# Optimization experiments

Measured on AMD Instinct MI355X. Metric: run time of the kernel, lower is better.

## Reference

```python
import jax, jax.numpy as jnp
import numpy as np

B, T, U, H, M, K, C = 64, 800, 80, 512, 20, 10, 80  # batch, tsteps, char len, rnn_size, nmixtures, kmixtures, char_vec_len


def _lstm(x, W, Uw, b):
    """Keras-semantics LSTM (gate order i,f,g,o), zero initial state. x: [B,T,D] -> [B,T,H]."""
    xg = jnp.einsum('btd,dh->bth', x, W) + b  # precompute input contribution
    h0 = jnp.zeros((x.shape[0], Uw.shape[0]), x.dtype)
    c0 = jnp.zeros_like(h0)

    def step(carry, zt):
        h, c = carry
        z = zt + h @ Uw
        i, f, g, o = jnp.split(z, 4, axis=-1)
        c = jax.nn.sigmoid(f) * c + jax.nn.sigmoid(i) * jnp.tanh(g)
        h = jax.nn.sigmoid(o) * jnp.tanh(c)
        return (h, c), h

    _, hs = jax.lax.scan(step, (h0, c0), jnp.swapaxes(xg, 0, 1))
    return jnp.swapaxes(hs, 0, 1)


def _forward(stroke_data, char_seq, kappa0, W0, U0, b0, W1, U1, b1, W2, U2, b2, Wa, ba, Wm, bm):
    lstm0_out = _lstm(stroke_data, W0, U0, b0)  # [B,T,H]
    # Attention window: the per-timestep loop in the source only carries kappa,
    # which is a running sum of exp(kappa_offset) -> vectorize via cumsum.
    abk = jnp.exp(jnp.einsum('bth,hk->btk', lstm0_out, Wa) + ba)  # [B,T,3K]
    alpha, beta, koff = jnpp_split = jnp.split(abk, 3, axis=-1)
    kappa = kappa0[:, None, :, 0] + jnp.cumsum(koff, axis=1)  # [B,T,K]
    u = jnp.arange(char_seq.shape[1], dtype=stroke_data.dtype)  # [U]
    # phi: [B,T,U] = sum_k alpha * exp(-beta * (kappa - u)^2)
    phi = jnp.sum(alpha[..., None] * jnp.exp(-beta[..., None] * (kappa[..., None] - u) ** 2), axis=2)
    windows = jnp.einsum('btu,buc->btc', phi, char_seq)  # [B,T,C]
    aug = jnp.concatenate([lstm0_out, windows, stroke_data], axis=-1)
    lstm1_out = _lstm(aug, W1, U1, b1)
    lstm2_out = _lstm(lstm1_out, W2, U2, b2)
    mdn = jnp.einsum('bth,hn->btn', lstm2_out, Wm) + bm  # [B,T,1+6M]
    eos_hat = mdn[..., 0:1]
    pi_hat, mu1, mu2, s1_hat, s2_hat, rho_hat = jnp.split(mdn[..., 1:], 6, axis=-1)
    return jnp.concatenate([
        jax.nn.sigmoid(-eos_hat),
        jax.nn.softmax(pi_hat, axis=-1),
        mu1, mu2,
        jnp.exp(s1_hat), jnp.exp(s2_hat),
        jnp.tanh(rho_hat),
    ], axis=-1)  # [B,T,1+6M]


def setup_inputs() -> dict:
    key = jax.random.key(0)
    ks = jax.random.split(key, 12)
    init = lambda k, shape: jax.random.truncated_normal(k, -2.0, 2.0, shape, jnp.float32) * 0.075
    return {
        'stroke_data': jax.random.normal(ks[0], (B, T, 3), jnp.float32),
        'char_seq': jax.nn.one_hot(jax.random.randint(ks[1], (B, U), 0, C), C, dtype=jnp.float32),
        'kappa0': jnp.zeros((B, K, 1), jnp.float32),
        'W0': init(ks[2], (3, 4 * H)), 'U0': init(ks[3], (H, 4 * H)), 'b0': jnp.zeros((4 * H,)),
        'W1': init(ks[4], (H + C + 3, 4 * H)), 'U1': init(ks[5], (H, 4 * H)), 'b1': jnp.zeros((4 * H,)),
        'W2': init(ks[6], (H, 4 * H)), 'U2': init(ks[7], (H, 4 * H)), 'b2': jnp.zeros((4 * H,)),
        'Wa': init(ks[8], (H, 3 * K)),
        'ba': -3.0 + 0.25 * jax.random.truncated_normal(ks[9], -2.0, 2.0, (3 * K,), jnp.float32),
        'Wm': init(ks[10], (H, 1 + 6 * M)), 'bm': jnp.zeros((1 + 6 * M,)),
    }


def reference(stroke_data, char_seq, kappa0, W0, U0, b0, W1, U1, b1, W2, U2, b2, Wa, ba, Wm, bm):
    return _forward(stroke_data, char_seq, kappa0, W0, U0, b0, W1, U1, b1, W2, U2, b2, Wa, ba, Wm, bm)
```

## Files before the change

### kernel.cpp

```cpp
#include <hip/hip_runtime.h>

typedef unsigned short u16;
typedef unsigned int u32;
typedef short v8s __attribute__((ext_vector_type(8)));
typedef float v4f __attribute__((ext_vector_type(4)));
typedef unsigned int v4u __attribute__((ext_vector_type(4)));
typedef unsigned int v2u __attribute__((ext_vector_type(2)));

#define MFMA16 __builtin_amdgcn_mfma_f32_16x16x32_bf16

constexpr int TT = 800;
constexpr int NBLK = 178;

constexpr int AUGB  = 2240;
constexpr int AUG2B = 2048;

constexpr size_t AUGR_OFF  = 16384;
constexpr size_t AUG2R_OFF = AUGR_OFF + (size_t)4 * 64 * AUGB;
constexpr size_t WAT_OFF   = AUG2R_OFF + (size_t)4 * 64 * AUG2B;
constexpr size_t WS_ZERO   = WAT_OFF + (size_t)32 * 512 * 2;

constexpr u32 SMEM_BYTES = 82944;

__device__ __forceinline__ float bf2f(u16 u) { return __uint_as_float(((u32)u) << 16); }
__device__ __forceinline__ u16 f2bf(float f) {
    u32 x = __float_as_uint(f);
    return (u16)((x + 0x7fffu + ((x >> 16) & 1u)) >> 16);
}
__device__ __forceinline__ short f2bfs(float f) { return (short)f2bf(f); }
__device__ __forceinline__ float sigf(float x) { return 1.f / (1.f + __expf(-x)); }
__device__ __forceinline__ float tanhf2(float x) { return 1.f - 2.f / (1.f + __expf(2.f * x)); }

__device__ __forceinline__ __amdgpu_buffer_rsrc_t mkrsrc(const void* p) {
    return __builtin_amdgcn_make_buffer_rsrc((void*)p, (short)0, -1, 0x00020000);
}
__device__ __forceinline__ v4u ldu4(__amdgpu_buffer_rsrc_t r, int off) {
    return __builtin_amdgcn_raw_buffer_load_b128(r, off, 0, 17);
}
__device__ __forceinline__ void stq8(__amdgpu_buffer_rsrc_t r, int off, u16 a, u16 b, u16 c, u16 d) {
    v2u t; t[0] = (u32)a | ((u32)b << 16); t[1] = (u32)c | ((u32)d << 16);
    __builtin_amdgcn_raw_buffer_store_b64(t, r, off, 0, 17);
}
__device__ __forceinline__ void stq4(__amdgpu_buffer_rsrc_t r, int off, u16 a, u16 b) {
    u32 t = (u32)a | ((u32)b << 16);
    __builtin_amdgcn_raw_buffer_store_b32(t, r, off, 0, 17);
}

__device__ __forceinline__ void gbar(u32* ctrl, u32 target) {
    __syncthreads();
    if (threadIdx.x == 0) {
        u32 old = __hip_atomic_fetch_add(ctrl, 1u, __ATOMIC_RELAXED, __HIP_MEMORY_SCOPE_AGENT);
        if (old == target * NBLK - 1) {
            #pragma unroll
            for (int k = 0; k < 32; k++)
                __hip_atomic_store(ctrl + 1024 + k * 64, target, __ATOMIC_RELAXED, __HIP_MEMORY_SCOPE_AGENT);
        } else {
            u32* gen = ctrl + 1024 + (blockIdx.x & 31) * 64;
            int sp = 0;
            while (__hip_atomic_load(gen, __ATOMIC_RELAXED, __HIP_MEMORY_SCOPE_AGENT) < target) {
                if (sp >= 2) __builtin_amdgcn_s_sleep(8);
                else if (sp == 1) __builtin_amdgcn_s_sleep(1);
                sp++;
            }
        }
    }
    __syncthreads();
}

__global__ void wat_init(const float* __restrict__ Wa, u16* __restrict__ WaT) {
    __amdgpu_buffer_rsrc_t r = mkrsrc(WaT);
    for (int idx = blockIdx.x * 256 + threadIdx.x; idx < 32 * 512 / 2; idx += gridDim.x * 256) {
        const int e0 = idx * 2, e1 = e0 + 1;
        const int n0 = e0 >> 9, k0 = e0 & 511;
        const int n1 = e1 >> 9, k1 = e1 & 511;
        const u16 a = (n0 < 30) ? f2bf(Wa[k0 * 30 + n0]) : (u16)0;
        const u16 b = (n1 < 30) ? f2bf(Wa[k1 * 30 + n1]) : (u16)0;
        stq4(r, idx * 4, a, b);
    }
}

__global__ __launch_bounds__(256, 1) void hw_main(
    const float* __restrict__ stroke, const float* __restrict__ charseq, const float* __restrict__ kappa0,
    const float* __restrict__ W0, const float* __restrict__ U0, const float* __restrict__ b0,
    const float* __restrict__ W1, const float* __restrict__ U1, const float* __restrict__ b1,
    const float* __restrict__ W2, const float* __restrict__ U2, const float* __restrict__ b2,
    const float* __restrict__ ba, const float* __restrict__ Wm, const float* __restrict__ bm,
    float* __restrict__ out, char* __restrict__ ws)
{
    extern __shared__ __align__(16) char smem[];
    u32* ctrl = (u32*)ws;
    u16* augr  = (u16*)(ws + AUGR_OFF);
    u16* aug2r = (u16*)(ws + AUG2R_OFF);
    const u16* WaT = (const u16*)(ws + WAT_OFF);

    const int blk = blockIdx.x, tid = threadIdx.x;
    const int wave = tid >> 6, lane = tid & 63;
    const int quad = lane >> 4, l15 = lane & 15;

    if (blk < 32) {
        const int cs = blk & 15, mg = blk >> 4;
        __amdgpu_buffer_rsrc_t ra = mkrsrc(augr);
        u16*   aL  = (u16*)smem;
        float* zb  = (float*)(smem + 33280);
        float* w0s = (float*)(smem + 50176);
        float* b0s = (float*)(smem + 51712);
        if (tid < 128) {
            const int cn2 = (tid >> 5) * 512 + cs * 32 + (tid & 31);
            b0s[tid] = b0[cn2];
            #pragma unroll
            for (int d = 0; d < 3; d++) w0s[d * 128 + tid] = W0[d * 2048 + cn2];
        }
        v8s bw0[16], bw1[16];
        {
            const int cnA = wave * 512 + cs * 32 + l15;
            const int cnB = cnA + 16;
            #pragma unroll
            for (int kc = 0; kc < 16; kc++)
                #pragma unroll
                for (int j = 0; j < 8; j++) {
                    const int k = kc * 32 + quad * 8 + j;
                    bw0[kc][j] = f2bfs(U0[k * 2048 + cnA]);
                    bw1[kc][j] = f2bfs(U0[k * 2048 + cnB]);
                }
        }
        float cst[4] = {0.f, 0.f, 0.f, 0.f};
        __syncthreads();
        #pragma unroll 1
        for (int i = 0; i <= TT + 3; i++) {
            if (i < TT) {
                const int t = i;
                {
                    const int base = (((t + 3) & 3) * 64 + mg * 32) * AUGB;
                    #pragma unroll
                    for (int c8 = 0; c8 < 8; c8++) {
                        const int c = tid + 256 * c8;
                        const int row = c >> 6, off = c & 63;
                        v4u d = ldu4(ra, base + row * AUGB + off * 16);
                        *(v4u*)((char*)aL + row * 1040 + off * 16) = d;
                    }
                }
                __syncthreads();
                v4f c0a = {0,0,0,0}, c0b = {0,0,0,0}, c1a = {0,0,0,0}, c1b = {0,0,0,0};
                const int xo = quad * 16;
                #pragma unroll
                for (int kc = 0; kc < 16; kc++) {
                    v8s x0 = *(const v8s*)((const char*)aL + l15 * 1040 + kc * 64 + xo);
                    v8s x1 = *(const v8s*)((const char*)aL + (16 + l15) * 1040 + kc * 64 + xo);
                    c0a = MFMA16(x0, bw0[kc], c0a, 0, 0, 0);
                    c1a = MFMA16(x0, bw1[kc], c1a, 0, 0, 0);
                    c0b = MFMA16(x1, bw0[kc], c0b, 0, 0, 0);
                    c1b = MFMA16(x1, bw1[kc], c1b, 0, 0, 0);
                }
                const int n0 = wave * 32 + l15, n1 = n0 + 16;
                #pragma unroll
                for (int r = 0; r < 4; r++) {
                    zb[(quad * 4 + r) * 132 + n0] = c0a[r];
                    zb[(quad * 4 + r) * 132 + n1] = c1a[r];
                    zb[(16 + quad * 4 + r) * 132 + n0] = c0b[r];
                    zb[(16 + quad * 4 + r) * 132 + n1] = c1b[r];
                }
                __syncthreads();
                {
                    const int bl = tid & 31, jj = tid >> 5;
                    const int b = mg * 32 + bl;
                    const float xx0 = stroke[(b * TT + t) * 3 + 0];
                    const float xx1 = stroke[(b * TT + t) * 3 + 1];
                    const float xx2 = stroke[(b * TT + t) * 3 + 2];
                    u16 hv[4];
                    #pragma unroll
                    for (int m = 0; m < 4; m++) {
                        const int j = jj * 4 + m;
                        float z[4];
                        #pragma unroll
                        for (int g = 0; g < 4; g++) {
                            const int n = g * 32 + j;
                            z[g] = zb[bl * 132 + n] + b0s[n] + xx0 * w0s[n] + xx1 * w0s[128 + n] + xx2 * w0s[256 + n];
                        }
                        const float cc = sigf(z[1]) * cst[m] + sigf(z[0]) * tanhf2(z[2]);
                        cst[m] = cc;
                        hv[m] = f2bf(sigf(z[3]) * tanhf2(cc));
                    }
                    stq8(ra, ((t & 3) * 64 + b) * AUGB + (cs * 32 + jj * 4) * 2, hv[0], hv[1], hv[2], hv[3]);
                }
            }
            if (i < TT + 3) gbar(ctrl, (u32)(i + 1));
        }
    } else if (blk < 96) {
        const int q = blk - 32, cs = q >> 1, mg = q & 1;
        __amdgpu_buffer_rsrc_t ra = mkrsrc(augr);
        __amdgpu_buffer_rsrc_t r2 = mkrsrc(aug2r);
        u16*   aL  = (u16*)smem;
        float* zb  = (float*)(smem + 72192);
        float* b1s = (float*)(smem + 80896);
        if (tid < 64) b1s[tid] = b1[(tid >> 4) * 512 + cs * 16 + (tid & 15)];
        v8s bw[35];
        {
            const int cn = wave * 512 + cs * 16 + l15;
            #pragma unroll
            for (int kc = 0; kc < 35; kc++)
                #pragma unroll
                for (int j = 0; j < 8; j++) {
                    const int k = kc * 32 + quad * 8 + j;
                    short v = 0;
                    if (k < 595) v = f2bfs(W1[k * 2048 + cn]);
                    else if (k >= 596 && k < 1108) v = f2bfs(U1[(k - 596) * 2048 + cn]);
                    bw[kc][j] = v;
                }
        }
        float cst[2] = {0.f, 0.f};
        __syncthreads();
        #pragma unroll 1
        for (int i = 0; i <= TT + 3; i++) {
            if (i >= 2 && i <= TT + 1) {
                const int t1 = i - 2;
                {
                    const int base = ((t1 & 3) * 64 + mg * 32) * AUGB;
                    #pragma unroll
                    for (int c18 = 0; c18 < 18; c18++) {
                        const int c = tid + 256 * c18;
                        if (c < 4480) {
                            const int row = c / 140, off = c - row * 140;
                            v4u d = ldu4(ra, base + row * AUGB + off * 16);
                            *(v4u*)((char*)aL + row * 2256 + off * 16) = d;
                        }
                    }
                }
                __syncthreads();
                v4f c0 = {0,0,0,0}, c1 = {0,0,0,0};
                const int xo = quad * 16;
                #pragma unroll
                for (int kc = 0; kc < 35; kc++) {
                    v8s x0 = *(const v8s*)((const char*)aL + l15 * 2256 + kc * 64 + xo);
                    v8s x1 = *(const v8s*)((const char*)aL + (16 + l15) * 2256 + kc * 64 + xo);
                    c0 = MFMA16(x0, bw[kc], c0, 0, 0, 0);
                    c1 = MFMA16(x1, bw[kc], c1, 0, 0, 0);
                }
                #pragma unroll
                for (int r = 0; r < 4; r++) {
                    zb[(quad * 4 + r) * 68 + wave * 17 + l15] = c0[r];
                    zb[(16 + quad * 4 + r) * 68 + wave * 17 + l15] = c1[r];
                }
                __syncthreads();
                {
                    const int bl = tid & 31, jj = tid >> 5;
                    const int b = mg * 32 + bl;
                    u16 hv[2];
                    #pragma unroll
                    for (int m = 0; m < 2; m++) {
                        const int j = jj * 2 + m;
                        float z[4];
                        #pragma unroll
                        for (int g = 0; g < 4; g++)
                            z[g] = zb[bl * 68 + g * 17 + j] + b1s[g * 16 + j];
                        const float cc = sigf(z[1]) * cst[m] + sigf(z[0]) * tanhf2(z[2]);
                        cst[m] = cc;
                        hv[m] = f2bf(sigf(z[3]) * tanhf2(cc));
                    }
                    stq4(ra, (((t1 + 1) & 3) * 64 + b) * AUGB + (596 + cs * 16 + jj * 2) * 2, hv[0], hv[1]);
                    stq4(r2, ((t1 & 3) * 64 + b) * AUG2B + (cs * 16 + jj * 2) * 2, hv[0], hv[1]);
                }
            }
            if (i < TT + 3) gbar(ctrl, (u32)(i + 1));
        }
    } else if (blk < 160) {
        const int q = blk - 96, cs = q >> 1, mg = q & 1;
        __amdgpu_buffer_rsrc_t r2 = mkrsrc(aug2r);
        u16*   aL  = (u16*)smem;
        float* zb  = (float*)(smem + 66048);
        float* b2s = (float*)(smem + 74752);
        if (tid < 64) b2s[tid] = b2[(tid >> 4) * 512 + cs * 16 + (tid & 15)];
        v8s bw[32];
        {
            const int cn = wave * 512 + cs * 16 + l15;
            #pragma unroll
            for (int kc = 0; kc < 32; kc++)
                #pragma unroll
                for (int j = 0; j < 8; j++) {
                    const int k = kc * 32 + quad * 8 + j;
                    bw[kc][j] = (k < 512) ? f2bfs(W2[k * 2048 + cn]) : f2bfs(U2[(k - 512) * 2048 + cn]);
                }
        }
        float cst[2] = {0.f, 0.f};
        __syncthreads();
        #pragma unroll 1
        for (int i = 0; i <= TT + 3; i++) {
            if (i >= 3 && i <= TT + 2) {
                const int t2 = i - 3;
                {
                    const int base = ((t2 & 3) * 64 + mg * 32) * AUG2B;
                    #pragma unroll
                    for (int c16 = 0; c16 < 16; c16++) {
                        const int c = tid + 256 * c16;
                        const int row = c >> 7, off = c & 127;
                        v4u d = ldu4(r2, base + row * AUG2B + off * 16);
                        *(v4u*)((char*)aL + row * 2064 + off * 16) = d;
                    }
                }
                __syncthreads();
                v4f c0 = {0,0,0,0}, c1 = {0,0,0,0};
                const int xo = quad * 16;
                #pragma unroll
                for (int kc = 0; kc < 32; kc++) {
                    v8s x0 = *(const v8s*)((const char*)aL + l15 * 2064 + kc * 64 + xo);
                    v8s x1 = *(const v8s*)((const char*)aL + (16 + l15) * 2064 + kc * 64 + xo);
                    c0 = MFMA16(x0, bw[kc], c0, 0, 0, 0);
                    c1 = MFMA16(x1, bw[kc], c1, 0, 0, 0);
                }
                #pragma unroll
                for (int r = 0; r < 4; r++) {
                    zb[(quad * 4 + r) * 68 + wave * 17 + l15] = c0[r];
                    zb[(16 + quad * 4 + r) * 68 + wave * 17 + l15] = c1[r];
                }
                __syncthreads();
                {
                    const int bl = tid & 31, jj = tid >> 5;
                    const int b = mg * 32 + bl;
                    u16 hv[2];
                    #pragma unroll
                    for (int m = 0; m < 2; m++) {
                        const int j = jj * 2 + m;
                        float z[4];
                        #pragma unroll
                        for (int g = 0; g < 4; g++)
                            z[g] = zb[bl * 68 + g * 17 + j] + b2s[g * 16 + j];
                        const float cc = sigf(z[1]) * cst[m] + sigf(z[0]) * tanhf2(z[2]);
                        cst[m] = cc;
                        hv[m] = f2bf(sigf(z[3]) * tanhf2(cc));
                    }
                    stq4(r2, (((t2 + 1) & 3) * 64 + b) * AUG2B + (512 + cs * 16 + jj * 2) * 2, hv[0], hv[1]);
                }
            }
            if (i < TT + 3) gbar(ctrl, (u32)(i + 1));
        }
    } else if (blk < 176) {
        const int a = blk - 160;
        const int b = a * 4 + wave;
        __amdgpu_buffer_rsrc_t ra = mkrsrc(augr);
        u16*   watl = (u16*)smem;
        u16*   hrow = (u16*)(smem + 33280);
        float* phis = (float*)(smem + 37440);
        u16*   idxs = (u16*)(smem + 38720);
        {
            #pragma unroll
            for (int c8 = 0; c8 < 8; c8++) {
                const int c = tid + 256 * c8;
                const int row = c >> 6, off = c & 63;
                *(v4u*)((char*)watl + row * 1040 + off * 16) = *(const v4u*)(WaT + row * 512 + off * 8);
            }
        }
        #pragma unroll
        for (int rep = 0; rep < 2; rep++) {
            const int u = rep * 64 + lane;
            if (u < 80) {
                int c = 0;
                #pragma unroll 1
                for (int cc = 0; cc < 80; cc++)
                    if (charseq[b * 6400 + u * 80 + cc] > 0.5f) c = cc;
                idxs[wave * 80 + u] = (u16)c;
            }
        }
        float kap = (lane < 10) ? kappa0[b * 10 + lane] : 0.f;
        const float baf = (lane < 30) ? ba[lane] : 0.f;
        const int nn = lane & 31;
        const int k0 = (lane >> 5) * 256;
        const u16* wrow = watl + nn * 520 + k0;
        __syncthreads();
        #pragma unroll 1
        for (int i = 0; i <= TT + 3; i++) {
            if (i >= 1 && i <= TT) {
                const int ta = i - 1;
                {
                    const int row = tid >> 6, off = tid & 63;
                    v4u d = ldu4(ra, ((ta & 3) * 64 + a * 4 + row) * AUGB + off * 16);
                    *(v4u*)((char*)hrow + row * 1040 + off * 16) = d;
                }
                __syncthreads();
                float acc = 0.f;
                #pragma unroll
                for (int kk = 0; kk < 32; kk++) {
                    v8s hv = *(const v8s*)((const char*)hrow + wave * 1040 + (k0 + kk * 8) * 2);
                    v8s wv = *(const v8s*)(wrow + kk * 8);
                    #pragma unroll
                    for (int e = 0; e < 8; e++) acc += bf2f((u16)hv[e]) * bf2f((u16)wv[e]);
                }
                acc += __shfl_xor(acc, 32);
                const float abk = __expf(acc + baf);
                const float kofv = __shfl(abk, 20 + (lane < 10 ? lane : 0));
                if (lane < 10) kap += kofv;
                const float u1f = (float)lane, u2f = (float)(64 + lane);
                float p1 = 0.f, p2 = 0.f;
                #pragma unroll
                for (int kk = 0; kk < 10; kk++) {
                    const float al = __shfl(abk, kk);
                    const float be = __shfl(abk, 10 + kk);
                    const float kp = __shfl(kap, kk);
                    const float d1 = kp - u1f, d2 = kp - u2f;
                    p1 += al * __expf(-be * d1 * d1);
                    p2 += al * __expf(-be * d2 * d2);
                }
                phis[wave * 80 + lane] = p1;
                if (lane < 16) phis[wave * 80 + 64 + lane] = p2;
                __syncthreads();
                const int db = (((ta & 3) * 64 + b) * AUGB) + 512 * 2;
                if (lane < 40) {
                    const int c0 = 2 * lane;
                    float w0 = 0.f, w1 = 0.f;
                    #pragma unroll 1
                    for (int u = 0; u < 80; u++) {
                        const float pv = phis[wave * 80 + u];
                        const int ix = (int)idxs[wave * 80 + u];
                        w0 += (ix == c0)     ? pv : 0.f;
                        w1 += (ix == c0 + 1) ? pv : 0.f;
                    }
                    stq4(ra, db + c0 * 2, f2bf(w0), f2bf(w1));
                } else if (lane == 40) {
                    stq4(ra, db + 80 * 2, f2bf(stroke[(b * TT + ta) * 3 + 0]), f2bf(stroke[(b * TT + ta) * 3 + 1]));
                } else if (lane == 41) {
                    stq4(ra, db + 82 * 2, f2bf(stroke[(b * TT + ta) * 3 + 2]), (u16)0);
                }
            }
            if (i < TT + 3) gbar(ctrl, (u32)(i + 1));
        }
    } else if (blk < 178) {
        const int mgs = blk - 176;
        __amdgpu_buffer_rsrc_t r2 = mkrsrc(aug2r);
        u16*   aL = (u16*)smem;
        float* zb = (float*)(smem + 33280);
        v8s bw0[16], bw1[16];
        {
            const int nA = wave * 32 + l15, nB = nA + 16;
            #pragma unroll
            for (int kc = 0; kc < 16; kc++)
                #pragma unroll
                for (int j = 0; j < 8; j++) {
                    const int k = kc * 32 + quad * 8 + j;
                    bw0[kc][j] = (nA < 121) ? f2bfs(Wm[k * 121 + nA]) : (short)0;
                    bw1[kc][j] = (nB < 121) ? f2bfs(Wm[k * 121 + nB]) : (short)0;
                }
        }
        __syncthreads();
        #pragma unroll 1
        for (int i = 0; i <= TT + 3; i++) {
            if (i >= 4) {
                const int tm = i - 4;
                {
                    const int base = (((tm + 1) & 3) * 64 + mgs * 32) * AUG2B + 1024;
                    #pragma unroll
                    for (int c8 = 0; c8 < 8; c8++) {
                        const int c = tid + 256 * c8;
                        const int row = c >> 6, off = c & 63;
                        v4u d = ldu4(r2, base + row * AUG2B + off * 16);
                        *(v4u*)((char*)aL + row * 1040 + off * 16) = d;
                    }
                }
                __syncthreads();
                v4f c0a = {0,0,0,0}, c0b = {0,0,0,0}, c1a = {0,0,0,0}, c1b = {0,0,0,0};
                const int xo = quad * 16;
                #pragma unroll
                for (int kc = 0; kc < 16; kc++) {
                    v8s x0 = *(const v8s*)((const char*)aL + l15 * 1040 + kc * 64 + xo);
                    v8s x1 = *(const v8s*)((const char*)aL + (16 + l15) * 1040 + kc * 64 + xo);
                    c0a = MFMA16(x0, bw0[kc], c0a, 0, 0, 0);
                    c1a = MFMA16(x0, bw1[kc], c1a, 0, 0, 0);
                    c0b = MFMA16(x1, bw0[kc], c0b, 0, 0, 0);
                    c1b = MFMA16(x1, bw1[kc], c1b, 0, 0, 0);
                }
                const int n0 = wave * 32 + l15, n1 = n0 + 16;
                #pragma unroll
                for (int r = 0; r < 4; r++) {
                    zb[(quad * 4 + r) * 132 + n0] = c0a[r];
                    zb[(quad * 4 + r) * 132 + n1] = c1a[r];
                    zb[(16 + quad * 4 + r) * 132 + n0] = c0b[r];
                    zb[(16 + quad * 4 + r) * 132 + n1] = c1b[r];
                }
                __syncthreads();
                {
                    const int b8 = tid >> 3, g8 = tid & 7;
                    const int b = mgs * 32 + b8;
                    const float* zr = zb + b8 * 132;
                    float* orow = out + ((size_t)(b * TT + tm)) * 121;
                    if (g8 == 0) {
                        orow[0] = sigf(-(zr[0] + bm[0]));
                        float mx = -1e30f;
                        float zv[20];
                        #pragma unroll 1
                        for (int nl = 1; nl <= 20; nl++) { zv[nl - 1] = zr[nl] + bm[nl]; mx = fmaxf(mx, zv[nl - 1]); }
                        float ss = 0.f;
                        #pragma unroll 1
                        for (int nl = 0; nl < 20; nl++) { zv[nl] = __expf(zv[nl] - mx); ss += zv[nl]; }
                        const float inv = 1.f / ss;
                        #pragma unroll 1
                        for (int nl = 0; nl < 20; nl++) orow[nl + 1] = zv[nl] * inv;
                    } else if (g8 <= 2) {
                        const int s0 = 21 + (g8 - 1) * 20;
                        #pragma unroll 1
                        for (int nl = s0; nl < s0 + 20; nl++) orow[nl] = zr[nl] + bm[nl];
                    } else if (g8 <= 4) {
                        const int s0 = 61 + (g8 - 3) * 20;
                        #pragma unroll 1
                        for (int nl = s0; nl < s0 + 20; nl++) orow[nl] = __expf(zr[nl] + bm[nl]);
                    } else if (g8 <= 6) {
                        const int s0 = 101 + (g8 - 5) * 10;
                        #pragma unroll 1
                        for (int nl = s0; nl < s0 + 10; nl++) orow[nl] = tanhf2(zr[nl] + bm[nl]);
                    }
                }
            }
            if (i < TT + 3) gbar(ctrl, (u32)(i + 1));
        }
    }
}

extern "C" void kernel_launch(void* const* d_in, const int* in_sizes, int n_in,
                              void* d_out, int out_size, void* d_ws, size_t ws_size,
                              hipStream_t stream) {
    const float* stroke  = (const float*)d_in[0];
    const float* charseq = (const float*)d_in[1];
    const float* kappa0  = (const float*)d_in[2];
    const float* W0 = (const float*)d_in[3];
    const float* U0 = (const float*)d_in[4];
    const float* b0 = (const float*)d_in[5];
    const float* W1 = (const float*)d_in[6];
    const float* U1 = (const float*)d_in[7];
    const float* b1 = (const float*)d_in[8];
    const float* W2 = (const float*)d_in[9];
    const float* U2 = (const float*)d_in[10];
    const float* b2 = (const float*)d_in[11];
    const float* Wa = (const float*)d_in[12];
    const float* ba = (const float*)d_in[13];
    const float* Wm = (const float*)d_in[14];
    const float* bm = (const float*)d_in[15];
    char* ws = (char*)d_ws;

    static bool attr_done = false;
    if (!attr_done) {
        hipFuncSetAttribute((const void*)hw_main,
                            hipFuncAttributeMaxDynamicSharedMemorySize, SMEM_BYTES);
        attr_done = true;
    }

    hipMemsetAsync(d_ws, 0, WS_ZERO, stream);
    wat_init<<<8, 256, 0, stream>>>(Wa, (u16*)(ws + WAT_OFF));
    hw_main<<<NBLK, 256, SMEM_BYTES, stream>>>(stroke, charseq, kappa0, W0, U0, b0,
                                               W1, U1, b1, W2, U2, b2, ba, Wm, bm,
                                               (float*)d_out, ws);
}
```

Measured before the change: 10.46 ms.

## Replace global lockstep barrier with per-stage dataflow counters between pipeline stages

Removes the grid-wide barrier that forced all 178 blocks to advance one step together. Each stage now publishes per-timestep completion counters, and before each step it waits only on the specific producer and consumer counters it depends on (done and read flags for a 4-slot ring). Stages can run ahead of each other and the critical recurrent path is no longer stalled by the slowest unrelated block. In exchange there are more atomics and polling per step, and the ring-buffer dependency logic has to be exactly right to avoid races.

Result: faster. 8.690 ms (-16.9%).

```diff
diff --git a/kernel.cpp b/kernel.cpp
--- a/kernel.cpp
+++ b/kernel.cpp
@@ -15,12 +15,14 @@
 constexpr int AUGB  = 2240;
 constexpr int AUG2B = 2048;
 
-constexpr size_t AUGR_OFF  = 16384;
+constexpr size_t AUGR_OFF  = 131072;
 constexpr size_t AUG2R_OFF = AUGR_OFF + (size_t)4 * 64 * AUGB;
 constexpr size_t WAT_OFF   = AUG2R_OFF + (size_t)4 * 64 * AUG2B;
 constexpr size_t WS_ZERO   = WAT_OFF + (size_t)32 * 512 * 2;
 
 constexpr u32 SMEM_BYTES = 82944;
+
+enum { G_S0D = 0, G_SAD = 1, G_S1D = 2, G_S2D = 3, G_S1R = 4, G_SAR = 5, G_S2R = 6, G_SMR = 7 };
 
 __device__ __forceinline__ float bf2f(u16 u) { return __uint_as_float(((u32)u) << 16); }
 __device__ __forceinline__ u16 f2bf(float f) {
@@ -46,22 +48,34 @@
     __builtin_amdgcn_raw_buffer_store_b32(t, r, off, 0, 17);
 }
 
-__device__ __forceinline__ void gbar(u32* ctrl, u32 target) {
-    __syncthreads();
-    if (threadIdx.x == 0) {
-        u32 old = __hip_atomic_fetch_add(ctrl, 1u, __ATOMIC_RELAXED, __HIP_MEMORY_SCOPE_AGENT);
-        if (old == target * NBLK - 1) {
-            #pragma unroll
-            for (int k = 0; k < 32; k++)
-                __hip_atomic_store(ctrl + 1024 + k * 64, target, __ATOMIC_RELAXED, __HIP_MEMORY_SCOPE_AGENT);
-        } else {
-            u32* gen = ctrl + 1024 + (blockIdx.x & 31) * 64;
-            int sp = 0;
-            while (__hip_atomic_load(gen, __ATOMIC_RELAXED, __HIP_MEMORY_SCOPE_AGENT) < target) {
-                if (sp >= 2) __builtin_amdgcn_s_sleep(8);
-                else if (sp == 1) __builtin_amdgcn_s_sleep(1);
-                sp++;
-            }
+__device__ __forceinline__ void publish(u32* ctrl, int g, int t, int blk) {
+    __hip_atomic_fetch_add(ctrl + g * 4096 + (t & 3) * 1024 + (blk & 15) * 64, 1u,
+                           __ATOMIC_RELAXED, __HIP_MEMORY_SCOPE_AGENT);
+}
+__device__ __forceinline__ void wait4(u32* ctrl,
+    int g0, int t0, u32 n0, int g1, int t1, u32 n1,
+    int g2, int t2, u32 n2, int g3, int t3, u32 n3)
+{
+    if (threadIdx.x < 64) {
+        const int lane = threadIdx.x;
+        const int cl = lane >> 4, k = lane & 15;
+        int g, tt; u32 nn;
+        if (cl == 0)      { g = g0; tt = t0; nn = n0; }
+        else if (cl == 1) { g = g1; tt = t1; nn = n1; }
+        else if (cl == 2) { g = g2; tt = t2; nn = n2; }
+        else              { g = g3; tt = t3; nn = n3; }
+        const u32 tgt = (g >= 0 && tt >= 0) ? nn * (u32)((tt >> 2) + 1) : 0u;
+        u32* p = (tgt > 0) ? (ctrl + g * 4096 + (tt & 3) * 1024 + k * 64) : (u32*)0;
+        int sp = 0;
+        for (;;) {
+            u32 v = p ? __hip_atomic_load(p, __ATOMIC_RELAXED, __HIP_MEMORY_SCOPE_AGENT) : 0u;
+            v += __shfl_xor(v, 1); v += __shfl_xor(v, 2);
+            v += __shfl_xor(v, 4); v += __shfl_xor(v, 8);
+            const bool bad = (tgt > 0) && (v < tgt);
+            if (__ballot(bad) == 0ull) break;
+            if (sp >= 2) __builtin_amdgcn_s_sleep(4);
+            else if (sp == 1) __builtin_amdgcn_s_sleep(1);
+            sp++;
         }
     }
     __syncthreads();
@@ -126,64 +140,63 @@
         float cst[4] = {0.f, 0.f, 0.f, 0.f};
         __syncthreads();
         #pragma unroll 1
-        for (int i = 0; i <= TT + 3; i++) {
-            if (i < TT) {
-                const int t = i;
-                {
-                    const int base = (((t + 3) & 3) * 64 + mg * 32) * AUGB;
+        for (int t = 0; t < TT; t++) {
+            wait4(ctrl, G_S0D, t - 1, 32, G_S1R, t - 4, 64, G_SAR, t - 4, 16, -1, 0, 0);
+            {
+                const int base = (((t + 3) & 3) * 64 + mg * 32) * AUGB;
+                #pragma unroll
+                for (int c8 = 0; c8 < 8; c8++) {
+                    const int c = tid + 256 * c8;
+                    const int row = c >> 6, off = c & 63;
+                    v4u d = ldu4(ra, base + row * AUGB + off * 16);
+                    *(v4u*)((char*)aL + row * 1040 + off * 16) = d;
+                }
+            }
+            __syncthreads();
+            v4f c0a = {0,0,0,0}, c0b = {0,0,0,0}, c1a = {0,0,0,0}, c1b = {0,0,0,0};
+            const int xo = quad * 16;
+            #pragma unroll
+            for (int kc = 0; kc < 16; kc++) {
+                v8s x0 = *(const v8s*)((const char*)aL + l15 * 1040 + kc * 64 + xo);
+                v8s x1 = *(const v8s*)((const char*)aL + (16 + l15) * 1040 + kc * 64 + xo);
+                c0a = MFMA16(x0, bw0[kc], c0a, 0, 0, 0);
+                c1a = MFMA16(x0, bw1[kc], c1a, 0, 0, 0);
+                c0b = MFMA16(x1, bw0[kc], c0b, 0, 0, 0);
+                c1b = MFMA16(x1, bw1[kc], c1b, 0, 0, 0);
+            }
+            const int n0 = wave * 32 + l15, n1 = n0 + 16;
+            #pragma unroll
+            for (int r = 0; r < 4; r++) {
+                zb[(quad * 4 + r) * 132 + n0] = c0a[r];
+                zb[(quad * 4 + r) * 132 + n1] = c1a[r];
+                zb[(16 + quad * 4 + r) * 132 + n0] = c0b[r];
+                zb[(16 + quad * 4 + r) * 132 + n1] = c1b[r];
+            }
+            __syncthreads();
+            {
+                const int bl = tid & 31, jj = tid >> 5;
+                const int b = mg * 32 + bl;
+                const float xx0 = stroke[(b * TT + t) * 3 + 0];
+                const float xx1 = stroke[(b * TT + t) * 3 + 1];
+                const float xx2 = stroke[(b * TT + t) * 3 + 2];
+                u16 hv[4];
+                #pragma unroll
+                for (int m = 0; m < 4; m++) {
+                    const int j = jj * 4 + m;
+                    float z[4];
                     #pragma unroll
-                    for (int c8 = 0; c8 < 8; c8++) {
-                        const int c = tid + 256 * c8;
-                        const int row = c >> 6, off = c & 63;
-                        v4u d = ldu4(ra, base + row * AUGB + off * 16);
-                        *(v4u*)((char*)aL + row * 1040 + off * 16) = d;
+                    for (int g = 0; g < 4; g++) {
+                        const int n = g * 32 + j;
+                        z[g] = zb[bl * 132 + n] + b0s[n] + xx0 * w0s[n] + xx1 * w0s[128 + n] + xx2 * w0s[256 + n];
                     }
-                }
-                __syncthreads();
-                v4f c0a = {0,0,0,0}, c0b = {0,0,0,0}, c1a = {0,0,0,0}, c1b = {0,0,0,0};
-                const int xo = quad * 16;
-                #pragma unroll
-                for (int kc = 0; kc < 16; kc++) {
-                    v8s x0 = *(const v8s*)((const char*)aL + l15 * 1040 + kc * 64 + xo);
-                    v8s x1 = *(const v8s*)((const char*)aL + (16 + l15) * 1040 + kc * 64 + xo);
-                    c0a = MFMA16(x0, bw0[kc], c0a, 0, 0, 0);
-                    c1a = MFMA16(x0, bw1[kc], c1a, 0, 0, 0);
-                    c0b = MFMA16(x1, bw0[kc], c0b, 0, 0, 0);
-                    c1b = MFMA16(x1, bw1[kc], c1b, 0, 0, 0);
-                }
-                const int n0 = wave * 32 + l15, n1 = n0 + 16;
-                #pragma unroll
-                for (int r = 0; r < 4; r++) {
-                    zb[(quad * 4 + r) * 132 + n0] = c0a[r];
-                    zb[(quad * 4 + r) * 132 + n1] = c1a[r];
-                    zb[(16 + quad * 4 + r) * 132 + n0] = c0b[r];
-                    zb[(16 + quad * 4 + r) * 132 + n1] = c1b[r];
-                }
-                __syncthreads();
-                {
-                    const int bl = tid & 31, jj = tid >> 5;
-                    const int b = mg * 32 + bl;
-                    const float xx0 = stroke[(b * TT + t) * 3 + 0];
-                    const float xx1 = stroke[(b * TT + t) * 3 + 1];
-                    const float xx2 = stroke[(b * TT + t) * 3 + 2];
-                    u16 hv[4];
-                    #pragma unroll
-                    for (int m = 0; m < 4; m++) {
-                        const int j = jj * 4 + m;
-                        float z[4];
-                        #pragma unroll
-                        for (int g = 0; g < 4; g++) {
-                            const int n = g * 32 + j;
-                            z[g] = zb[bl * 132 + n] + b0s[n] + xx0 * w0s[n] + xx1 * w0s[128 + n] + xx2 * w0s[256 + n];
-                        }
-                        const float cc = sigf(z[1]) * cst[m] + sigf(z[0]) * tanhf2(z[2]);
-                        cst[m] = cc;
-                        hv[m] = f2bf(sigf(z[3]) * tanhf2(cc));
-                    }
-                    stq8(ra, ((t & 3) * 64 + b) * AUGB + (cs * 32 + jj * 4) * 2, hv[0], hv[1], hv[2], hv[3]);
-                }
-            }
-            if (i < TT + 3) gbar(ctrl, (u32)(i + 1));
+                    const float cc = sigf(z[1]) * cst[m] + sigf(z[0]) * tanhf2(z[2]);
+                    cst[m] = cc;
+                    hv[m] = f2bf(sigf(z[3]) * tanhf2(cc));
+                }
+                stq8(ra, ((t & 3) * 64 + b) * AUGB + (cs * 32 + jj * 4) * 2, hv[0], hv[1], hv[2], hv[3]);
+            }
+            __syncthreads();
+            if (tid == 0) publish(ctrl, G_S0D, t, blk);
         }
     } else if (blk < 96) {
         const int q = blk - 32, cs = q >> 1, mg = q & 1;
@@ -210,57 +223,57 @@
         float cst[2] = {0.f, 0.f};
         __syncthreads();
         #pragma unroll 1
-        for (int i = 0; i <= TT + 3; i++) {
-            if (i >= 2 && i <= TT + 1) {
-                const int t1 = i - 2;
-                {
-                    const int base = ((t1 & 3) * 64 + mg * 32) * AUGB;
+        for (int t = 0; t < TT; t++) {
+            wait4(ctrl, G_S0D, t, 32, G_SAD, t, 16, G_S1D, t - 1, 64, G_S2R, t - 4, 64);
+            {
+                const int base = ((t & 3) * 64 + mg * 32) * AUGB;
+                #pragma unroll
+                for (int c18 = 0; c18 < 18; c18++) {
+                    const int c = tid + 256 * c18;
+                    if (c < 4480) {
+                        const int row = c / 140, off = c - row * 140;
+                        v4u d = ldu4(ra, base + row * AUGB + off * 16);
+                        *(v4u*)((char*)aL + row * 2256 + off * 16) = d;
+                    }
+                }
+            }
+            __syncthreads();
+            if (tid == 0) publish(ctrl, G_S1R, t, blk);
+            v4f c0 = {0,0,0,0}, c1 = {0,0,0,0};
+            const int xo = quad * 16;
+            #pragma unroll
+            for (int kc = 0; kc < 35; kc++) {
+                v8s x0 = *(const v8s*)((const char*)aL + l15 * 2256 + kc * 64 + xo);
+                v8s x1 = *(const v8s*)((const char*)aL + (16 + l15) * 2256 + kc * 64 + xo);
+                c0 = MFMA16(x0, bw[kc], c0, 0, 0, 0);
+                c1 = MFMA16(x1, bw[kc], c1, 0, 0, 0);
+            }
+            #pragma unroll
+            for (int r = 0; r < 4; r++) {
+                zb[(quad * 4 + r) * 68 + wave * 17 + l15] = c0[r];
+                zb[(16 + quad * 4 + r) * 68 + wave * 17 + l15] = c1[r];
+            }
+            __syncthreads();
+            {
+                const int bl = tid & 31, jj = tid >> 5;
+                const int b = mg * 32 + bl;
+                u16 hv[2];
+                #pragma unroll
+                for (int m = 0; m < 2; m++) {
+                    const int j = jj * 2 + m;
+                    float z[4];
                     #pragma unroll
-                    for (int c18 = 0; c18 < 18; c18++) {
-                        const int c = tid + 256 * c18;
-                        if (c < 4480) {
-                            const int row = c / 140, off = c - row * 140;
-                            v4u d = ldu4(ra, base + row * AUGB + off * 16);
-                            *(v4u*)((char*)aL + row * 2256 + off * 16) = d;
-                        }
-                    }
-                }
-                __syncthreads();
-                v4f c0 = {0,0,0,0}, c1 = {0,0,0,0};
-                const int xo = quad * 16;
-                #pragma unroll
-                for (int kc = 0; kc < 35; kc++) {
-                    v8s x0 = *(const v8s*)((const char*)aL + l15 * 2256 + kc * 64 + xo);
-                    v8s x1 = *(const v8s*)((const char*)aL + (16 + l15) * 2256 + kc * 64 + xo);
-                    c0 = MFMA16(x0, bw[kc], c0, 0, 0, 0);
-                    c1 = MFMA16(x1, bw[kc], c1, 0, 0, 0);
-                }
-                #pragma unroll
-                for (int r = 0; r < 4; r++) {
-                    zb[(quad * 4 + r) * 68 + wave * 17 + l15] = c0[r];
-                    zb[(16 + quad * 4 + r) * 68 + wave * 17 + l15] = c1[r];
-                }
-                __syncthreads();
-                {
-                    const int bl = tid & 31, jj = tid >> 5;
-                    const int b = mg * 32 + bl;
-                    u16 hv[2];
-                    #pragma unroll
-                    for (int m = 0; m < 2; m++) {
-                        const int j = jj * 2 + m;
-                        float z[4];
-                        #pragma unroll
-                        for (int g = 0; g < 4; g++)
-                            z[g] = zb[bl * 68 + g * 17 + j] + b1s[g * 16 + j];
-                        const float cc = sigf(z[1]) * cst[m] + sigf(z[0]) * tanhf2(z[2]);
-                        cst[m] = cc;
-                        hv[m] = f2bf(sigf(z[3]) * tanhf2(cc));
-                    }
-                    stq4(ra, (((t1 + 1) & 3) * 64 + b) * AUGB + (596 + cs * 16 + jj * 2) * 2, hv[0], hv[1]);
-                    stq4(r2, ((t1 & 3) * 64 + b) * AUG2B + (cs * 16 + jj * 2) * 2, hv[0], hv[1]);
-                }
-            }
-            if (i < TT + 3) gbar(ctrl, (u32)(i + 1));
+                    for (int g = 0; g < 4; g++)
+                        z[g] = zb[bl * 68 + g * 17 + j] + b1s[g * 16 + j];
+                    const float cc = sigf(z[1]) * cst[m] + sigf(z[0]) * tanhf2(z[2]);
+                    cst[m] = cc;
+                    hv[m] = f2bf(sigf(z[3]) * tanhf2(cc));
+                }
+                stq4(ra, (((t + 1) & 3) * 64 + b) * AUGB + (596 + cs * 16 + jj * 2) * 2, hv[0], hv[1]);
+                stq4(r2, ((t & 3) * 64 + b) * AUG2B + (cs * 16 + jj * 2) * 2, hv[0], hv[1]);
+            }
+            __syncthreads();
+            if (tid == 0) publish(ctrl, G_S1D, t, blk);
         }
     } else if (blk < 160) {
         const int q = blk - 96, cs = q >> 1, mg = q & 1;
@@ -283,54 +296,54 @@
         float cst[2] = {0.f, 0.f};
         __syncthreads();
         #pragma unroll 1
-        for (int i = 0; i <= TT + 3; i++) {
-            if (i >= 3 && i <= TT + 2) {
-                const int t2 = i - 3;
-                {
-                    const int base = ((t2 & 3) * 64 + mg * 32) * AUG2B;
+        for (int t = 0; t < TT; t++) {
+            wait4(ctrl, G_S1D, t, 64, G_S2D, t - 1, 64, G_SMR, t - 4, 2, -1, 0, 0);
+            {
+                const int base = ((t & 3) * 64 + mg * 32) * AUG2B;
+                #pragma unroll
+                for (int c16 = 0; c16 < 16; c16++) {
+                    const int c = tid + 256 * c16;
+                    const int row = c >> 7, off = c & 127;
+                    v4u d = ldu4(r2, base + row * AUG2B + off * 16);
+                    *(v4u*)((char*)aL + row * 2064 + off * 16) = d;
+                }
+            }
+            __syncthreads();
+            if (tid == 0) publish(ctrl, G_S2R, t, blk);
+            v4f c0 = {0,0,0,0}, c1 = {0,0,0,0};
+            const int xo = quad * 16;
+            #pragma unroll
+            for (int kc = 0; kc < 32; kc++) {
+                v8s x0 = *(const v8s*)((const char*)aL + l15 * 2064 + kc * 64 + xo);
+                v8s x1 = *(const v8s*)((const char*)aL + (16 + l15) * 2064 + kc * 64 + xo);
+                c0 = MFMA16(x0, bw[kc], c0, 0, 0, 0);
+                c1 = MFMA16(x1, bw[kc], c1, 0, 0, 0);
+            }
+            #pragma unroll
+            for (int r = 0; r < 4; r++) {
+                zb[(quad * 4 + r) * 68 + wave * 17 + l15] = c0[r];
+                zb[(16 + quad * 4 + r) * 68 + wave * 17 + l15] = c1[r];
+            }
+            __syncthreads();
+            {
+                const int bl = tid & 31, jj = tid >> 5;
+                const int b = mg * 32 + bl;
+                u16 hv[2];
+                #pragma unroll
+                for (int m = 0; m < 2; m++) {
+                    const int j = jj * 2 + m;
+                    float z[4];
                     #pragma unroll
-                    for (int c16 = 0; c16 < 16; c16++) {
-                        const int c = tid + 256 * c16;
-                        const int row = c >> 7, off = c & 127;
-                        v4u d = ldu4(r2, base + row * AUG2B + off * 16);
-                        *(v4u*)((char*)aL + row * 2064 + off * 16) = d;
-                    }
-                }
-                __syncthreads();
-                v4f c0 = {0,0,0,0}, c1 = {0,0,0,0};
-                const int xo = quad * 16;
-                #pragma unroll
-                for (int kc = 0; kc < 32; kc++) {
-                    v8s x0 = *(const v8s*)((const char*)aL + l15 * 2064 + kc * 64 + xo);
-                    v8s x1 = *(const v8s*)((const char*)aL + (16 + l15) * 2064 + kc * 64 + xo);
-                    c0 = MFMA16(x0, bw[kc], c0, 0, 0, 0);
-                    c1 = MFMA16(x1, bw[kc], c1, 0, 0, 0);
-                }
-                #pragma unroll
-                for (int r = 0; r < 4; r++) {
-                    zb[(quad * 4 + r) * 68 + wave * 17 + l15] = c0[r];
-                    zb[(16 + quad * 4 + r) * 68 + wave * 17 + l15] = c1[r];
-                }
-                __syncthreads();
-                {
-                    const int bl = tid & 31, jj = tid >> 5;
-                    const int b = mg * 32 + bl;
-                    u16 hv[2];
-                    #pragma unroll
-                    for (int m = 0; m < 2; m++) {
-                        const int j = jj * 2 + m;
-                        float z[4];
-                        #pragma unroll
-                        for (int g = 0; g < 4; g++)
-                            z[g] = zb[bl * 68 + g * 17 + j] + b2s[g * 16 + j];
-                        const float cc = sigf(z[1]) * cst[m] + sigf(z[0]) * tanhf2(z[2]);
-                        cst[m] = cc;
-                        hv[m] = f2bf(sigf(z[3]) * tanhf2(cc));
-                    }
-                    stq4(r2, (((t2 + 1) & 3) * 64 + b) * AUG2B + (512 + cs * 16 + jj * 2) * 2, hv[0], hv[1]);
-                }
-            }
-            if (i < TT + 3) gbar(ctrl, (u32)(i + 1));
+                    for (int g = 0; g < 4; g++)
+                        z[g] = zb[bl * 68 + g * 17 + j] + b2s[g * 16 + j];
+                    const float cc = sigf(z[1]) * cst[m] + sigf(z[0]) * tanhf2(z[2]);
+                    cst[m] = cc;
+                    hv[m] = f2bf(sigf(z[3]) * tanhf2(cc));
+                }
+                stq4(r2, (((t + 1) & 3) * 64 + b) * AUG2B + (512 + cs * 16 + jj * 2) * 2, hv[0], hv[1]);
+            }
+            __syncthreads();
+            if (tid == 0) publish(ctrl, G_S2D, t, blk);
         }
     } else if (blk < 176) {
         const int a = blk - 160;
@@ -366,62 +379,62 @@
         const u16* wrow = watl + nn * 520 + k0;
         __syncthreads();
         #pragma unroll 1
-        for (int i = 0; i <= TT + 3; i++) {
-            if (i >= 1 && i <= TT) {
-                const int ta = i - 1;
-                {
-                    const int row = tid >> 6, off = tid & 63;
-                    v4u d = ldu4(ra, ((ta & 3) * 64 + a * 4 + row) * AUGB + off * 16);
-                    *(v4u*)((char*)hrow + row * 1040 + off * 16) = d;
-                }
-                __syncthreads();
-                float acc = 0.f;
-                #pragma unroll
-                for (int kk = 0; kk < 32; kk++) {
-                    v8s hv = *(const v8s*)((const char*)hrow + wave * 1040 + (k0 + kk * 8) * 2);
-                    v8s wv = *(const v8s*)(wrow + kk * 8);
-                    #pragma unroll
-                    for (int e = 0; e < 8; e++) acc += bf2f((u16)hv[e]) * bf2f((u16)wv[e]);
-                }
-                acc += __shfl_xor(acc, 32);
-                const float abk = __expf(acc + baf);
-                const float kofv = __shfl(abk, 20 + (lane < 10 ? lane : 0));
-                if (lane < 10) kap += kofv;
-                const float u1f = (float)lane, u2f = (float)(64 + lane);
-                float p1 = 0.f, p2 = 0.f;
-                #pragma unroll
-                for (int kk = 0; kk < 10; kk++) {
-                    const float al = __shfl(abk, kk);
-                    const float be = __shfl(abk, 10 + kk);
-                    const float kp = __shfl(kap, kk);
-                    const float d1 = kp - u1f, d2 = kp - u2f;
-                    p1 += al * __expf(-be * d1 * d1);
-                    p2 += al * __expf(-be * d2 * d2);
-                }
-                phis[wave * 80 + lane] = p1;
-                if (lane < 16) phis[wave * 80 + 64 + lane] = p2;
-                __syncthreads();
-                const int db = (((ta & 3) * 64 + b) * AUGB) + 512 * 2;
-                if (lane < 40) {
-                    const int c0 = 2 * lane;
-                    float w0 = 0.f, w1 = 0.f;
-                    #pragma unroll 1
-                    for (int u = 0; u < 80; u++) {
-                        const float pv = phis[wave * 80 + u];
-                        const int ix = (int)idxs[wave * 80 + u];
-                        w0 += (ix == c0)     ? pv : 0.f;
-                        w1 += (ix == c0 + 1) ? pv : 0.f;
-                    }
-                    stq4(ra, db + c0 * 2, f2bf(w0), f2bf(w1));
-                } else if (lane == 40) {
-                    stq4(ra, db + 80 * 2, f2bf(stroke[(b * TT + ta) * 3 + 0]), f2bf(stroke[(b * TT + ta) * 3 + 1]));
-                } else if (lane == 41) {
-                    stq4(ra, db + 82 * 2, f2bf(stroke[(b * TT + ta) * 3 + 2]), (u16)0);
-                }
-            }
-            if (i < TT + 3) gbar(ctrl, (u32)(i + 1));
-        }
-    } else if (blk < 178) {
+        for (int t = 0; t < TT; t++) {
+            wait4(ctrl, G_S0D, t, 32, G_S1R, t - 4, 64, -1, 0, 0, -1, 0, 0);
+            {
+                const int row = tid >> 6, off = tid & 63;
+                v4u d = ldu4(ra, ((t & 3) * 64 + a * 4 + row) * AUGB + off * 16);
+                *(v4u*)((char*)hrow + row * 1040 + off * 16) = d;
+            }
+            __syncthreads();
+            if (tid == 0) publish(ctrl, G_SAR, t, blk);
+            float acc = 0.f;
+            #pragma unroll
+            for (int kk = 0; kk < 32; kk++) {
+                v8s hv = *(const v8s*)((const char*)hrow + wave * 1040 + (k0 + kk * 8) * 2);
+                v8s wv = *(const v8s*)(wrow + kk * 8);
+                #pragma unroll
+                for (int e = 0; e < 8; e++) acc += bf2f((u16)hv[e]) * bf2f((u16)wv[e]);
+            }
+            acc += __shfl_xor(acc, 32);
+            const float abk = __expf(acc + baf);
+            const float kofv = __shfl(abk, 20 + (lane < 10 ? lane : 0));
+            if (lane < 10) kap += kofv;
+            const float u1f = (float)lane;
+            float p1 = 0.f, p2 = 0.f;
+            #pragma unroll
+            for (int kk = 0; kk < 10; kk++) {
+                const float al = __shfl(abk, kk);
+                const float be = __shfl(abk, 10 + kk);
+                const float kp = __shfl(kap, kk);
+                const float d1 = kp - u1f, d2 = kp - (u1f + 64.f);
+                p1 += al * __expf(-be * d1 * d1);
+                p2 += al * __expf(-be * d2 * d2);
+            }
+            phis[wave * 80 + lane] = p1;
+            if (lane < 16) phis[wave * 80 + 64 + lane] = p2;
+            __syncthreads();
+            const int db = (((t & 3) * 64 + b) * AUGB) + 512 * 2;
+            if (lane < 40) {
+                const int c0 = 2 * lane;
+                float w0 = 0.f, w1 = 0.f;
+                #pragma unroll 1
+                for (int u = 0; u < 80; u++) {
+                    const float pv = phis[wave * 80 + u];
+                    const int ix = (int)idxs[wave * 80 + u];
+                    w0 += (ix == c0)     ? pv : 0.f;
+                    w1 += (ix == c0 + 1) ? pv : 0.f;
+                }
+                stq4(ra, db + c0 * 2, f2bf(w0), f2bf(w1));
+            } else if (lane == 40) {
+                stq4(ra, db + 80 * 2, f2bf(stroke[(b * TT + t) * 3 + 0]), f2bf(stroke[(b * TT + t) * 3 + 1]));
+            } else if (lane == 41) {
+                stq4(ra, db + 82 * 2, f2bf(stroke[(b * TT + t) * 3 + 2]), (u16)0);
+            }
+            __syncthreads();
+            if (tid == 0) publish(ctrl, G_SAD, t, blk);
+        }
+    } else {
         const int mgs = blk - 176;
         __amdgpu_buffer_rsrc_t r2 = mkrsrc(aug2r);
         u16*   aL = (u16*)smem;
@@ -440,73 +453,72 @@
         }
         __syncthreads();
         #pragma unroll 1
-        for (int i = 0; i <= TT + 3; i++) {
-            if (i >= 4) {
-                const int tm = i - 4;
-                {
-                    const int base = (((tm + 1) & 3) * 64 + mgs * 32) * AUG2B + 1024;
-                    #pragma unroll
-                    for (int c8 = 0; c8 < 8; c8++) {
-                        const int c = tid + 256 * c8;
-                        const int row = c >> 6, off = c & 63;
-                        v4u d = ldu4(r2, base + row * AUG2B + off * 16);
-                        *(v4u*)((char*)aL + row * 1040 + off * 16) = d;
-                    }
-                }
-                __syncthreads();
-                v4f c0a = {0,0,0,0}, c0b = {0,0,0,0}, c1a = {0,0,0,0}, c1b = {0,0,0,0};
-                const int xo = quad * 16;
-                #pragma unroll
-                for (int kc = 0; kc < 16; kc++) {
-                    v8s x0 = *(const v8s*)((const char*)aL + l15 * 1040 + kc * 64 + xo);
-                    v8s x1 = *(const v8s*)((const char*)aL + (16 + l15) * 1040 + kc * 64 + xo);
-                    c0a = MFMA16(x0, bw0[kc], c0a, 0, 0, 0);
-                    c1a = MFMA16(x0, bw1[kc], c1a, 0, 0, 0);
-                    c0b = MFMA16(x1, bw0[kc], c0b, 0, 0, 0);
-                    c1b = MFMA16(x1, bw1[kc], c1b, 0, 0, 0);
-                }
-                const int n0 = wave * 32 + l15, n1 = n0 + 16;
-                #pragma unroll
-                for (int r = 0; r < 4; r++) {
-                    zb[(quad * 4 + r) * 132 + n0] = c0a[r];
-                    zb[(quad * 4 + r) * 132 + n1] = c1a[r];
-                    zb[(16 + quad * 4 + r) * 132 + n0] = c0b[r];
-                    zb[(16 + quad * 4 + r) * 132 + n1] = c1b[r];
-                }
-                __syncthreads();
-                {
-                    const int b8 = tid >> 3, g8 = tid & 7;
-                    const int b = mgs * 32 + b8;
-                    const float* zr = zb + b8 * 132;
-                    float* orow = out + ((size_t)(b * TT + tm)) * 121;
-                    if (g8 == 0) {
-                        orow[0] = sigf(-(zr[0] + bm[0]));
-                        float mx = -1e30f;
-                        float zv[20];
-                        #pragma unroll 1
-                        for (int nl = 1; nl <= 20; nl++) { zv[nl - 1] = zr[nl] + bm[nl]; mx = fmaxf(mx, zv[nl - 1]); }
-                        float ss = 0.f;
-                        #pragma unroll 1
-                        for (int nl = 0; nl < 20; nl++) { zv[nl] = __expf(zv[nl] - mx); ss += zv[nl]; }
-                        const float inv = 1.f / ss;
-                        #pragma unroll 1
-                        for (int nl = 0; nl < 20; nl++) orow[nl + 1] = zv[nl] * inv;
-                    } else if (g8 <= 2) {
-                        const int s0 = 21 + (g8 - 1) * 20;
-                        #pragma unroll 1
-                        for (int nl = s0; nl < s0 + 20; nl++) orow[nl] = zr[nl] + bm[nl];
-                    } else if (g8 <= 4) {
-                        const int s0 = 61 + (g8 - 3) * 20;
-                        #pragma unroll 1
-                        for (int nl = s0; nl < s0 + 20; nl++) orow[nl] = __expf(zr[nl] + bm[nl]);
-                    } else if (g8 <= 6) {
-                        const int s0 = 101 + (g8 - 5) * 10;
-                        #pragma unroll 1
-                        for (int nl = s0; nl < s0 + 10; nl++) orow[nl] = tanhf2(zr[nl] + bm[nl]);
-                    }
-                }
-            }
-            if (i < TT + 3) gbar(ctrl, (u32)(i + 1));
+        for (int t = 0; t < TT; t++) {
+            wait4(ctrl, G_S2D, t, 64, -1, 0, 0, -1, 0, 0, -1, 0, 0);
+            {
+                const int base = (((t + 1) & 3) * 64 + mgs * 32) * AUG2B + 1024;
+                #pragma unroll
+                for (int c8 = 0; c8 < 8; c8++) {
+                    const int c = tid + 256 * c8;
+                    const int row = c >> 6, off = c & 63;
+                    v4u d = ldu4(r2, base + row * AUG2B + off * 16);
+                    *(v4u*)((char*)aL + row * 1040 + off * 16) = d;
+                }
+            }
+            __syncthreads();
+            if (tid == 0) publish(ctrl, G_SMR, t, blk);
+            v4f c0a = {0,0,0,0}, c0b = {0,0,0,0}, c1a = {0,0,0,0}, c1b = {0,0,0,0};
+            const int xo = quad * 16;
+            #pragma unroll
+            for (int kc = 0; kc < 16; kc++) {
+                v8s x0 = *(const v8s*)((const char*)aL + l15 * 1040 + kc * 64 + xo);
+                v8s x1 = *(const v8s*)((const char*)aL + (16 + l15) * 1040 + kc * 64 + xo);
+                c0a = MFMA16(x0, bw0[kc], c0a, 0, 0, 0);
+                c1a = MFMA16(x0, bw1[kc], c1a, 0, 0, 0);
+                c0b = MFMA16(x1, bw0[kc], c0b, 0, 0, 0);
+                c1b = MFMA16(x1, bw1[kc], c1b, 0, 0, 0);
+            }
+            const int n0 = wave * 32 + l15, n1 = n0 + 16;
+            #pragma unroll
+            for (int r = 0; r < 4; r++) {
+                zb[(quad * 4 + r) * 132 + n0] = c0a[r];
+                zb[(quad * 4 + r) * 132 + n1] = c1a[r];
+                zb[(16 + quad * 4 + r) * 132 + n0] = c0b[r];
+                zb[(16 + quad * 4 + r) * 132 + n1] = c1b[r];
+            }
+            __syncthreads();
+            {
+                const int b8 = tid >> 3, g8 = tid & 7;
+                const int b = mgs * 32 + b8;
+                const float* zr = zb + b8 * 132;
+                float* orow = out + ((size_t)(b * TT + t)) * 121;
+                if (g8 == 0) {
+                    orow[0] = sigf(-(zr[0] + bm[0]));
+                    float mx = -1e30f;
+                    float zv[20];
+                    #pragma unroll 1
+                    for (int nl = 1; nl <= 20; nl++) { zv[nl - 1] = zr[nl] + bm[nl]; mx = fmaxf(mx, zv[nl - 1]); }
+                    float ss = 0.f;
+                    #pragma unroll 1
+                    for (int nl = 0; nl < 20; nl++) { zv[nl] = __expf(zv[nl] - mx); ss += zv[nl]; }
+                    const float inv = 1.f / ss;
+                    #pragma unroll 1
+                    for (int nl = 0; nl < 20; nl++) orow[nl + 1] = zv[nl] * inv;
+                } else if (g8 <= 2) {
+                    const int s0 = 21 + (g8 - 1) * 20;
+                    #pragma unroll 1
+                    for (int nl = s0; nl < s0 + 20; nl++) orow[nl] = zr[nl] + bm[nl];
+                } else if (g8 <= 4) {
+                    const int s0 = 61 + (g8 - 3) * 20;
+                    #pragma unroll 1
+                    for (int nl = s0; nl < s0 + 20; nl++) orow[nl] = __expf(zr[nl] + bm[nl]);
+                } else if (g8 <= 6) {
+                    const int s0 = 101 + (g8 - 5) * 10;
+                    #pragma unroll 1
+                    for (int nl = s0; nl < s0 + 10; nl++) orow[nl] = tanhf2(zr[nl] + bm[nl]);
+                }
+            }
+            __syncthreads();
         }
     }
 }
```
